# Optimization experiments

Hardware: AMD Instinct MI355X
Metric: run time of the kernel (lower is better)

Reference implementation:

```python
import jax, jax.numpy as jnp
import numpy as np

EPS = 1e-6

def rms_norm(x):
    # RMSNorm, affine=False
    return x * jax.lax.rsqrt(jnp.mean(x * x, axis=-1, keepdims=True) + EPS)

def apply_rope(x, cos, sin):
    # x: [N, T, h, d], cos/sin: [T, d//2], half-split rotation
    x1, x2 = jnp.split(x, 2, axis=-1)
    c = cos[None, :, None, :]
    s = sin[None, :, None, :]
    return jnp.concatenate([x1 * c - x2 * s, x1 * s + x2 * c], axis=-1)

def setup_inputs() -> dict:
    key = jax.random.key(0)
    k0, k1, k2 = jax.random.split(key, 3)
    N, T, D, hd = 1, 2048, 2048, 128
    input_NTD = jax.random.normal(k0, (N, T, D), jnp.float32)
    qkv_weight = jax.random.normal(k1, (3, D, D), jnp.float32) / np.sqrt(D) / 2.0
    o_weight = jax.random.normal(k2, (D, D), jnp.float32) * 0.02
    # standard 1d RoPE angle table
    pos = jnp.arange(T, dtype=jnp.float32)
    inv_freq = 1.0 / (10000.0 ** (jnp.arange(hd // 2, dtype=jnp.float32) / (hd // 2)))
    ang = pos[:, None] * inv_freq[None, :]  # [T, hd//2]
    return {
        "input_NTD": input_NTD,
        "qkv_weight": qkv_weight,
        "o_weight": o_weight,
        "cos": jnp.cos(ang),
        "sin": jnp.sin(ang),
    }

def reference(input_NTD, qkv_weight, o_weight, cos, sin):
    N, T, D = input_NTD.shape
    hd = cos.shape[-1] * 2
    h = D // hd
    w = qkv_weight.reshape(3 * D, D)
    qkv = rms_norm(input_NTD) @ w.T                      # [N, T, 3D]
    qkv = qkv.reshape(N, T, 3 * h, hd)
    q, k, v = jnp.split(qkv, 3, axis=2)                  # each [N, T, h, hd]
    q = apply_rope(rms_norm(q), cos, sin)
    k = apply_rope(rms_norm(k), cos, sin)
    scale = 1.0 / np.sqrt(hd)
    scores = jnp.einsum('nqhd,nkhd->nhqk', q, k) * scale  # [N, h, T, T]
    causal = jnp.tril(jnp.ones((T, T), bool))
    scores = jnp.where(causal[None, None], scores, -jnp.inf)
    att = jax.nn.softmax(scores, axis=-1)
    x = jnp.einsum('nhqk,nkhd->nqhd', att, v).reshape(N, T, D)
    out = input_NTD + x @ o_weight.T
    return out, k, v
```

## Files before the change

### kernel.cpp

```cpp
#include <hip/hip_runtime.h>
#include <hip/hip_bf16.h>

typedef unsigned short u16;
typedef unsigned int u32;
typedef __bf16 bf16x8 __attribute__((ext_vector_type(8)));
typedef u16 u16x8 __attribute__((ext_vector_type(8)));
typedef u16 u16x4 __attribute__((ext_vector_type(4)));
typedef float f32x4 __attribute__((ext_vector_type(4)));

#define T_SEQ 2048
#define DMODEL 2048
#define NHEAD 16
#define HDIM 128
#define ATT_SCALE 0.08838834764831843f

__device__ __forceinline__ u16 f2bf(float f) {
    return __builtin_bit_cast(u16, __float2bfloat16(f));
}
__device__ __forceinline__ bf16x8 as_bf(u16x8 v) {
    return __builtin_bit_cast(bf16x8, v);
}
__device__ __forceinline__ float lo2f(u32 w) { return __builtin_bit_cast(float, w << 16); }
__device__ __forceinline__ float hi2f(u32 w) { return __builtin_bit_cast(float, w & 0xffff0000u); }
__device__ __forceinline__ float bf2f(u16 v) { return __builtin_bit_cast(float, (u32)v << 16); }
__device__ __forceinline__ void gload_lds16(const u16* g, u16* l) {
    __builtin_amdgcn_global_load_lds(
        (const __attribute__((address_space(1))) u32*)(g),
        (__attribute__((address_space(3))) u32*)(l), 16, 0, 0);
}

__global__ __launch_bounds__(256) void prep(const float* __restrict__ w1,
                                            const float* __restrict__ w2,
                                            const float* __restrict__ x,
                                            u16* __restrict__ d1,
                                            u16* __restrict__ d2,
                                            u16* __restrict__ xn) {
    const int b = blockIdx.x, tid = threadIdx.x;
    if (b < 8192) {
        int i = b * 256 + tid;
        const float* src; u16* dst; int k;
        if (i < 1572864) { src = w1; dst = d1; k = i; }
        else             { src = w2; dst = d2; k = i - 1572864; }
        float4 a = ((const float4*)src)[2 * k];
        float4 bb = ((const float4*)src)[2 * k + 1];
        u16x8 o;
        o[0] = f2bf(a.x); o[1] = f2bf(a.y); o[2] = f2bf(a.z); o[3] = f2bf(a.w);
        o[4] = f2bf(bb.x); o[5] = f2bf(bb.y); o[6] = f2bf(bb.z); o[7] = f2bf(bb.w);
        *(u16x8*)(dst + (size_t)k * 8) = o;
        return;
    }
    const int row = b - 8192;
    const float* xr = x + (size_t)row * DMODEL;
    float4 a = ((const float4*)xr)[2 * tid];
    float4 bb = ((const float4*)xr)[2 * tid + 1];
    float ss = a.x*a.x + a.y*a.y + a.z*a.z + a.w*a.w
             + bb.x*bb.x + bb.y*bb.y + bb.z*bb.z + bb.w*bb.w;
#pragma unroll
    for (int off = 32; off; off >>= 1) ss += __shfl_xor(ss, off);
    __shared__ float red[4];
    if ((tid & 63) == 0) red[tid >> 6] = ss;
    __syncthreads();
    float tot = red[0] + red[1] + red[2] + red[3];
    float r = rsqrtf(tot * (1.f / DMODEL) + 1e-6f);
    u16x8 o;
    o[0] = f2bf(a.x*r); o[1] = f2bf(a.y*r); o[2] = f2bf(a.z*r); o[3] = f2bf(a.w*r);
    o[4] = f2bf(bb.x*r); o[5] = f2bf(bb.y*r); o[6] = f2bf(bb.z*r); o[7] = f2bf(bb.w*r);
    *(u16x8*)(xn + (size_t)row * DMODEL + tid * 8) = o;
}

#define VM2 asm volatile("s_waitcnt vmcnt(2)" ::: "memory");
#define VM4 asm volatile("s_waitcnt vmcnt(4)" ::: "memory");
#define VM0 asm volatile("s_waitcnt vmcnt(0)" ::: "memory");

#define ENDP                                                                  \
  __builtin_amdgcn_s_barrier();                                               \
  __builtin_amdgcn_sched_barrier(0);

#define LDA6(DST, BUF, MH)                                                    \
  _Pragma("unroll") for (int mq = 0; mq < 4; ++mq) {                          \
    int ra = wr + (MH) * 64 + mq * 16 + fr;                                   \
    int sw = ra & 7;                                                          \
    _Pragma("unroll") for (int k2 = 0; k2 < 2; ++k2)                          \
      DST[mq][k2] = *(const u16x8*)(sA[BUF] + ra * 64 +                       \
                                    ((((k2 << 2) | fg) ^ sw) << 3));          \
  }

#define LDB0_192(BUF)                                                         \
  _Pragma("unroll") for (int nq = 0; nq < 2; ++nq) {                          \
    int rb = wc + nq * 16 + fr;                                               \
    int sw = rb & 7;                                                          \
    _Pragma("unroll") for (int k2 = 0; k2 < 2; ++k2)                          \
      bv[nq][k2] = *(const u16x8*)(sB[BUF] + rb * 64 +                        \
                                   ((((k2 << 2) | fg) ^ sw) << 3));           \
  }

#define LDB1_192(BUF)                                                         \
  {                                                                           \
    int rb = wc + 32 + fr;                                                    \
    int sw = rb & 7;                                                          \
    _Pragma("unroll") for (int k2 = 0; k2 < 2; ++k2)                          \
      bv1[k2] = *(const u16x8*)(sB[BUF] + rb * 64 +                           \
                                ((((k2 << 2) | fg) ^ sw) << 3));              \
  }

#define MN0(AV, MH)                                                           \
  __builtin_amdgcn_s_barrier();                                               \
  __builtin_amdgcn_s_setprio(1);                                              \
  _Pragma("unroll") for (int k2 = 0; k2 < 2; ++k2)                            \
    _Pragma("unroll") for (int mq = 0; mq < 4; ++mq)                          \
      _Pragma("unroll") for (int nq = 0; nq < 2; ++nq)                        \
        acc[(MH) * 4 + mq][nq] = __builtin_amdgcn_mfma_f32_16x16x32_bf16(     \
            as_bf(AV[mq][k2]), as_bf(bv[nq][k2]), acc[(MH) * 4 + mq][nq],     \
            0, 0, 0);                                                         \
  __builtin_amdgcn_s_setprio(0);

#define MN1B                                                                  \
  __builtin_amdgcn_s_barrier();                                               \
  __builtin_amdgcn_s_setprio(1);                                              \
  _Pragma("unroll") for (int k2 = 0; k2 < 2; ++k2)                            \
    _Pragma("unroll") for (int mq = 0; mq < 4; ++mq) {                        \
      acc[mq][2] = __builtin_amdgcn_mfma_f32_16x16x32_bf16(                   \
          as_bf(av[mq][k2]), as_bf(bv1[k2]), acc[mq][2], 0, 0, 0);            \
      acc[4 + mq][2] = __builtin_amdgcn_mfma_f32_16x16x32_bf16(               \
          as_bf(av2[mq][k2]), as_bf(bv1[k2]), acc[4 + mq][2], 0, 0, 0);       \
    }                                                                         \
  __builtin_amdgcn_s_setprio(0);

__global__ __launch_bounds__(512) void gemm192(const u16* __restrict__ A,
                                               const u16* __restrict__ B,
                                               u16* __restrict__ C,
                                               int M, int N, int K) {
    extern __shared__ char smem[];
    const int tid = threadIdx.x, lane = tid & 63, wid = tid >> 6;
    const int bm = blockIdx.y * 256, bn = blockIdx.x * 192;
    const int wr = (wid >> 2) * 128, wc = (wid & 3) * 48;
    const int fr = lane & 15, fg = lane >> 4;

    u16* sA[2] = {(u16*)smem, (u16*)(smem + 57344)};
    u16* sB[2] = {(u16*)(smem + 32768), (u16*)(smem + 90112)};

    const int cs = (((tid & 7) ^ ((tid >> 3) & 7)) << 3);
    const int s8 = (tid & 7) << 3;
    const int rr6 = tid >> 3;

    auto stA = [&](int buf, int k0, int mh) {
#pragma unroll
        for (int j = 0; j < 2; ++j) {
            int r = j * 128 + mh * 64 + rr6;
            gload_lds16(A + (size_t)(bm + r) * K + k0 + cs, sA[buf] + r * 64 + s8);
        }
    };
    auto stB = [&](int buf, int k0, int bt) {
        int r = bt * 64 + rr6;
        gload_lds16(B + (size_t)(bn + r) * K + k0 + cs, sB[buf] + r * 64 + s8);
    };

    f32x4 acc[8][3] = {};
    u16x8 av[4][2], av2[4][2], bv[2][2], bv1[2];
    const int nt = K >> 6;

    stA(0, 0, 0); stA(0, 0, 1); stB(0, 0, 0); stB(0, 0, 1); stB(0, 0, 2);
    stA(1, 64, 0); stA(1, 64, 1);
    VM4
    __builtin_amdgcn_s_barrier();
    __builtin_amdgcn_sched_barrier(0);

    for (int it = 0; it < (nt >> 1); ++it) {
        const int kc = it << 7;
        const int kn1 = kc + 64, kn2 = kc + 128, kn3 = kc + 192;
        const bool st2 = (kn2 < K), st3 = (kn3 < K);

        LDA6(av, 0, 0) LDB0_192(0)
        stB(1, kn1, 0); stB(1, kn1, 1);
        MN0(av, 0) ENDP
        LDB1_192(0) LDA6(av2, 0, 1)
        stB(1, kn1, 2);
        if (st2) stA(0, kn2, 0);
        MN1B ENDP
        if (st2) stA(0, kn2, 1);
        MN0(av2, 1)
        if (st2) { VM4 } else { VM0 }
        ENDP
        LDA6(av, 1, 0) LDB0_192(1)
        if (st2) { stB(0, kn2, 0); stB(0, kn2, 1); }
        MN0(av, 0) ENDP
        LDB1_192(1) LDA6(av2, 1, 1)
        if (st2) stB(0, kn2, 2);
        if (st3) stA(1, kn3, 0);
        MN1B ENDP
        if (st3) stA(1, kn3, 1);
        MN0(av2, 1)
        if (st3) { VM4 } else { VM0 }
        ENDP
    }

#pragma unroll
    for (int am = 0; am < 8; ++am)
#pragma unroll
        for (int bq = 0; bq < 3; ++bq)
#pragma unroll
            for (int r = 0; r < 4; ++r) {
                int row = bm + wr + am * 16 + fg * 4 + r;
                int col = bn + wc + bq * 16 + fr;
                C[(size_t)row * N + col] = f2bf(acc[am][bq][r]);
            }
}

#define LDAH(BUF, MH)                                                         \
  _Pragma("unroll") for (int mq = 0; mq < 2; ++mq) {                          \
    int ra = wr + (MH) * 32 + mq * 16 + fr;                                   \
    int sw = ra & 7;                                                          \
    _Pragma("unroll") for (int k2 = 0; k2 < 2; ++k2)                          \
      avh[mq][k2] = *(const u16x8*)(sA[BUF] + ra * 64 +                       \
                                    ((((k2 << 2) | fg) ^ sw) << 3));          \
  }

#define LDBH(BUF, NH)                                                         \
  _Pragma("unroll") for (int nq = 0; nq < 2; ++nq) {                          \
    int rb = wc + (NH) * 32 + nq * 16 + fr;                                   \
    int sw = rb & 7;                                                          \
    _Pragma("unroll") for (int k2 = 0; k2 < 2; ++k2)                          \
      bvh[nq][k2] = *(const u16x8*)(sB[BUF] + rb * 64 +                       \
                                    ((((k2 << 2) | fg) ^ sw) << 3));          \
  }

#define MFMAQH(MH, NH)                                                        \
  __builtin_amdgcn_s_barrier();                                               \
  __builtin_amdgcn_s_setprio(1);                                              \
  _Pragma("unroll") for (int k2 = 0; k2 < 2; ++k2)                            \
    _Pragma("unroll") for (int mq = 0; mq < 2; ++mq)                          \
      _Pragma("unroll") for (int nq = 0; nq < 2; ++nq)                        \
        acc[(MH) * 2 + mq][(NH) * 2 + nq] =                                   \
            __builtin_amdgcn_mfma_f32_16x16x32_bf16(                          \
                as_bf(avh[mq][k2]), as_bf(bvh[nq][k2]),                       \
                acc[(MH) * 2 + mq][(NH) * 2 + nq], 0, 0, 0);                  \
  __builtin_amdgcn_s_setprio(0);

__global__ __launch_bounds__(256) void gemm128(const u16* __restrict__ A,
                                               const u16* __restrict__ B,
                                               float* __restrict__ C,
                                               const float* __restrict__ resid,
                                               int M, int N, int K) {
    extern __shared__ char smem[];
    const int tid = threadIdx.x, lane = tid & 63, wid = tid >> 6;
    const int bm = blockIdx.y * 128, bn = blockIdx.x * 128;
    const int wr = (wid >> 1) * 64, wc = (wid & 1) * 64;
    const int fr = lane & 15, fg = lane >> 4;

    u16* sA[2] = {(u16*)smem, (u16*)(smem + 32768)};
    u16* sB[2] = {(u16*)(smem + 16384), (u16*)(smem + 49152)};

    const int cs = (((tid & 7) ^ ((tid >> 3) & 7)) << 3);
    const int s8 = (tid & 7) << 3;
    const int rr5 = tid >> 3;

    auto stA = [&](int buf, int k0, int mh) {
#pragma unroll
        for (int j = 0; j < 2; ++j) {
            int r = j * 64 + mh * 32 + rr5;
            gload_lds16(A + (size_t)(bm + r) * K + k0 + cs, sA[buf] + r * 64 + s8);
        }
    };
    auto stB = [&](int buf, int k0, int nh) {
#pragma unroll
        for (int j = 0; j < 2; ++j) {
            int r = j * 64 + nh * 32 + rr5;
            gload_lds16(B + (size_t)(bn + r) * K + k0 + cs, sB[buf] + r * 64 + s8);
        }
    };

    f32x4 acc[4][4] = {};
    u16x8 avh[2][2], bvh[2][2];
    const int nt = K >> 6;

    stA(0, 0, 0); stA(0, 0, 1); stB(0, 0, 0); stB(0, 0, 1);
    stA(1, 64, 0); stB(1, 64, 1);
    VM4
    __builtin_amdgcn_s_barrier();
    __builtin_amdgcn_sched_barrier(0);

    for (int it = 0; it < (nt >> 1); ++it) {
        const int kc = it << 7;
        const int kn1 = kc + 64, kn2 = kc + 128, kn3 = kc + 192;
        const bool st2 = (kn2 < K), st3 = (kn3 < K);

        LDAH(0, 0) LDBH(0, 0)
        stA(1, kn1, 1);
        MFMAQH(0, 0) ENDP
        LDBH(0, 1)
        stB(1, kn1, 0);
        MFMAQH(0, 1) ENDP
        LDAH(0, 1)
        if (st2) stA(0, kn2, 0);
        MFMAQH(1, 1) ENDP
        LDBH(0, 0)
        if (st2) stB(0, kn2, 1);
        MFMAQH(1, 0)
        if (st2) { VM4 } else { VM0 }
        ENDP
        LDAH(1, 0) LDBH(1, 0)
        if (st2) stA(0, kn2, 1);
        MFMAQH(0, 0) ENDP
        LDBH(1, 1)
        if (st2) stB(0, kn2, 0);
        MFMAQH(0, 1) ENDP
        LDAH(1, 1)
        if (st3) stA(1, kn3, 0);
        MFMAQH(1, 1) ENDP
        LDBH(1, 0)
        if (st3) stB(1, kn3, 1);
        MFMAQH(1, 0)
        VM4
        ENDP
    }

#pragma unroll
    for (int am = 0; am < 4; ++am)
#pragma unroll
        for (int bq = 0; bq < 4; ++bq)
#pragma unroll
            for (int r = 0; r < 4; ++r) {
                int row = bm + wr + am * 16 + fg * 4 + r;
                int col = bn + wc + bq * 16 + fr;
                float val = acc[am][bq][r] + resid[(size_t)row * N + col];
                C[(size_t)row * N + col] = val;
            }
}

__global__ __launch_bounds__(256) void rope_split(const u16* __restrict__ qkv,
                                                  const float* __restrict__ cosb,
                                                  const float* __restrict__ sinb,
                                                  u16* __restrict__ q_bf,
                                                  u16* __restrict__ k_bf,
                                                  float* __restrict__ k_out,
                                                  float* __restrict__ v_out) {
    const int t = blockIdx.x, tid = threadIdx.x, wid = tid >> 6, lane = tid & 63;
    const u16* row = qkv + (size_t)t * (3 * DMODEL);
    const int dp = (lane & 31) << 1;
    float2 c2 = *(const float2*)(cosb + t * 64 + dp);
    float2 s2 = *(const float2*)(sinb + t * 64 + dp);
    const bool hi = lane >= 32;

    for (int task = wid; task < 32; task += 4) {
        u32 w = *(const u32*)(row + task * 128 + lane * 2);
        float xa = lo2f(w), xb = hi2f(w);
        float ss = xa * xa + xb * xb;
#pragma unroll
        for (int off = 32; off; off >>= 1) ss += __shfl_xor(ss, off);
        float rn = rsqrtf(ss * (1.f / 128.f) + 1e-6f);
        float pa = __shfl_xor(xa, 32), pb = __shfl_xor(xb, 32);
        float oa, ob;
        if (!hi) {
            oa = (xa * c2.x - pa * s2.x) * rn;
            ob = (xb * c2.y - pb * s2.y) * rn;
        } else {
            oa = (pa * s2.x + xa * c2.x) * rn;
            ob = (pb * s2.y + xb * c2.y) * rn;
        }
        u32 pk = (u32)f2bf(oa) | ((u32)f2bf(ob) << 16);
        if (task < 16) {
            *(u32*)(q_bf + ((size_t)task * T_SEQ + t) * 128 + lane * 2) = pk;
        } else {
            int hh = task - 16;
            *(u32*)(k_bf + ((size_t)hh * T_SEQ + t) * 128 + lane * 2) = pk;
            float2 kk; kk.x = oa; kk.y = ob;
            *(float2*)(k_out + (size_t)t * DMODEL + hh * 128 + lane * 2) = kk;
        }
    }
    {
        u16x8 vv = *(const u16x8*)(row + 2 * DMODEL + tid * 8);
        float4 f0, f1;
        f0.x = bf2f(vv[0]); f0.y = bf2f(vv[1]); f0.z = bf2f(vv[2]); f0.w = bf2f(vv[3]);
        f1.x = bf2f(vv[4]); f1.y = bf2f(vv[5]); f1.z = bf2f(vv[6]); f1.w = bf2f(vv[7]);
        *(float4*)(v_out + (size_t)t * DMODEL + tid * 8) = f0;
        *(float4*)(v_out + (size_t)t * DMODEL + tid * 8 + 4) = f1;
    }
}

__global__ __launch_bounds__(256) void vtrans(const u16* __restrict__ qkv,
                                              u16* __restrict__ vt) {
    const int b = blockIdx.x, tid = threadIdx.x;
    const int head = b >> 7;
    const int i = (b & 127) * 256 + tid;
    const int d = i & 127, tc = i >> 7;
    u16x8 o;
#pragma unroll
    for (int j = 0; j < 8; ++j)
        o[j] = qkv[(size_t)(tc * 8 + j) * (3 * DMODEL) + 2 * DMODEL + head * 128 + d];
    *(u16x8*)&vt[((size_t)head * 128 + d) * T_SEQ + tc * 8] = o;
}

__global__ __launch_bounds__(256) void attn_part(const u16* __restrict__ qb,
                                                 const u16* __restrict__ kb,
                                                 const u16* __restrict__ vtb,
                                                 u16* __restrict__ opart,
                                                 float* __restrict__ ml) {
    __shared__ u16 Ks[64 * 128];
    __shared__ u16 Vs[128 * 64];
    __shared__ u16 Ps[4][16 * 64];

    const int bid = blockIdx.x;
    const int r8 = bid & 7, s = bid >> 3;
    const int hs = s >> 6, g = (s >> 5) & 1, m = s & 31;
    const int head = r8 + (hs << 3);
    const int qt = g ? (31 - m) : m;
    const int nt = qt + 1;
    const int h0c = (nt + 1) >> 1;
    const int first = g ? h0c : 0;
    const int count = g ? (nt - h0c) : h0c;
    const int pidx = (head * 32 + qt) * 2 + g;

    const int tid = threadIdx.x, wid = tid >> 6, lane = tid & 63;
    const int fr = lane & 15, fg = lane >> 4;
    const u16* kh = kb + (size_t)head * T_SEQ * 128;
    const u16* vth = vtb + (size_t)head * 128 * T_SEQ;
    const u16* qh = qb + (size_t)head * T_SEQ * 128;
    const int q0 = qt * 64 + wid * 16;
    const int qrow_g = q0 + fr;

    u16x8 bq[4];
    {
        const u16* qrow = qh + (size_t)(q0 + fr) * 128 + fg * 8;
#pragma unroll
        for (int cc = 0; cc < 4; ++cc) bq[cc] = *(const u16x8*)(qrow + cc * 32);
    }

    auto stage = [&](int kv0) {
#pragma unroll
        for (int i = 0; i < 4; ++i) {
            int idx = i * 256 + tid;
            int r = idx >> 4;
            int cbs = ((idx & 15) << 4) ^ ((r & 7) << 4);
            gload_lds16(kh + (size_t)(kv0 + r) * 128 + (cbs >> 1), &Ks[idx * 8]);
        }
#pragma unroll
        for (int i = 0; i < 4; ++i) {
            int idx = i * 256 + tid;
            int d = idx >> 3;
            int cbs = ((idx & 7) << 4) ^ ((d & 7) << 4);
            gload_lds16(vth + (size_t)d * T_SEQ + kv0 + (cbs >> 1), &Vs[idx * 8]);
        }
    };

    f32x4 o[8] = {};
    float m_run = -1e30f, l_run = 0.f;

    for (int i = 0; i < count; ++i) {
        const int kv0 = (first + i) * 64;
        stage(kv0);
        asm volatile("s_waitcnt vmcnt(0)" ::: "memory");
        __builtin_amdgcn_s_barrier();
        __builtin_amdgcn_sched_barrier(0);

        const char* ksb = (const char*)&Ks[0];
        const char* vsb = (const char*)&Vs[0];
        char* psb = (char*)&Ps[wid][0];

        float p[4][4];
        float mx = -1e30f;
        const bool diag = (kv0 + 64 > q0);
#pragma unroll
        for (int st = 0; st < 4; ++st) {
            f32x4 sacc = {0.f, 0.f, 0.f, 0.f};
#pragma unroll
            for (int c4 = 0; c4 < 4; ++c4) {
                int r = st * 16 + fr;
                int cb = c4 * 64 + fg * 16;
                u16x8 ak = *(const u16x8*)(ksb + r * 256 + (cb ^ ((r & 7) << 4)));
                sacc = __builtin_amdgcn_mfma_f32_16x16x32_bf16(
                    as_bf(ak), as_bf(bq[c4]), sacc, 0, 0, 0);
            }
#pragma unroll
            for (int rr = 0; rr < 4; ++rr) {
                float sv = sacc[rr] * ATT_SCALE;
                if (diag) {
                    int kvg = kv0 + st * 16 + fg * 4 + rr;
                    sv = (kvg <= qrow_g) ? sv : -1e30f;
                }
                p[st][rr] = sv;
                mx = fmaxf(mx, sv);
            }
        }
        mx = fmaxf(mx, __shfl_xor(mx, 16));
        mx = fmaxf(mx, __shfl_xor(mx, 32));

        if (__all(mx - m_run <= 8.f)) {
            float rs = 0.f;
#pragma unroll
            for (int st = 0; st < 4; ++st) {
                u16x4 pw;
#pragma unroll
                for (int rr = 0; rr < 4; ++rr) {
                    float e = __expf(p[st][rr] - m_run);
                    rs += e;
                    pw[rr] = f2bf(e);
                }
                *(u16x4*)(psb + fr * 128 + ((st * 32 + fg * 8) ^ ((fr & 7) << 4))) = pw;
            }
            rs += __shfl_xor(rs, 16);
            rs += __shfl_xor(rs, 32);
            l_run += rs;
        } else {
            float m_new = fmaxf(m_run, mx);
            float corr = __expf(m_run - m_new);
            float rs = 0.f;
#pragma unroll
            for (int st = 0; st < 4; ++st) {
                u16x4 pw;
#pragma unroll
                for (int rr = 0; rr < 4; ++rr) {
                    float e = __expf(p[st][rr] - m_new);
                    rs += e;
                    pw[rr] = f2bf(e);
                }
                *(u16x4*)(psb + fr * 128 + ((st * 32 + fg * 8) ^ ((fr & 7) << 4))) = pw;
            }
            rs += __shfl_xor(rs, 16);
            rs += __shfl_xor(rs, 32);
            l_run = l_run * corr + rs;
            m_run = m_new;
            float ct[4];
#pragma unroll
            for (int rr = 0; rr < 4; ++rr) ct[rr] = __shfl(corr, fg * 4 + rr);
#pragma unroll
            for (int f = 0; f < 8; ++f)
#pragma unroll
                for (int rr = 0; rr < 4; ++rr) o[f][rr] *= ct[rr];
        }

#pragma unroll
        for (int ks = 0; ks < 2; ++ks) {
            u16x8 pa = *(const u16x8*)(psb + fr * 128 + ((ks * 64 + fg * 16) ^ ((fr & 7) << 4)));
#pragma unroll
            for (int f = 0; f < 8; ++f) {
                int d = f * 16 + fr;
                u16x8 vB = *(const u16x8*)(vsb + d * 128 + ((ks * 64 + fg * 16) ^ ((d & 7) << 4)));
                o[f] = __builtin_amdgcn_mfma_f32_16x16x32_bf16(
                    as_bf(pa), as_bf(vB), o[f], 0, 0, 0);
            }
        }
        __builtin_amdgcn_s_barrier();
        __builtin_amdgcn_sched_barrier(0);
    }

    u16* op = opart + (size_t)pidx * 8192;
#pragma unroll
    for (int f = 0; f < 8; ++f)
#pragma unroll
        for (int rr = 0; rr < 4; ++rr)
            op[(wid * 16 + fg * 4 + rr) * 128 + f * 16 + fr] = f2bf(o[f][rr]);
    if (fg == 0) {
        ml[pidx * 128 + wid * 16 + fr] = m_run;
        ml[pidx * 128 + 64 + wid * 16 + fr] = l_run;
    }
}

__global__ __launch_bounds__(256) void attn_merge(const u16* __restrict__ opart,
                                                  const float* __restrict__ ml,
                                                  u16* __restrict__ xout) {
    const int b = blockIdx.x, tid = threadIdx.x;
    const int head = b >> 5, qt = b & 31;
    const int p0 = b * 2, p1 = b * 2 + 1;
    const int row = tid >> 2, d0 = (tid & 3) * 32;

    float m0 = ml[p0 * 128 + row], l0 = ml[p0 * 128 + 64 + row];
    float m1 = ml[p1 * 128 + row], l1 = ml[p1 * 128 + 64 + row];
    float M = fmaxf(m0, m1);
    float w0 = __expf(m0 - M), w1 = __expf(m1 - M);
    float inv = 1.f / (l0 * w0 + l1 * w1);
    w0 *= inv; w1 *= inv;

    const u16* a0 = opart + (size_t)p0 * 8192 + row * 128 + d0;
    const u16* a1 = opart + (size_t)p1 * 8192 + row * 128 + d0;
    u16* dst = xout + (size_t)(qt * 64 + row) * DMODEL + head * 128 + d0;
#pragma unroll
    for (int j = 0; j < 4; ++j) {
        u16x8 v0 = *(const u16x8*)(a0 + j * 8);
        u16x8 v1 = *(const u16x8*)(a1 + j * 8);
        u16x8 ov;
#pragma unroll
        for (int e = 0; e < 8; ++e)
            ov[e] = f2bf(bf2f(v0[e]) * w0 + bf2f(v1[e]) * w1);
        *(u16x8*)(dst + j * 8) = ov;
    }
}

extern "C" void kernel_launch(void* const* d_in, const int* in_sizes, int n_in,
                              void* d_out, int out_size, void* d_ws, size_t ws_size,
                              hipStream_t stream) {
    const float* x_in = (const float*)d_in[0];
    const float* w_qkv = (const float*)d_in[1];
    const float* w_o = (const float*)d_in[2];
    const float* cosb = (const float*)d_in[3];
    const float* sinb = (const float*)d_in[4];

    float* out = (float*)d_out;
    float* k_out = out + 4194304;
    float* v_out = out + 8388608;

    char* ws = (char*)d_ws;
    u16* xn    = (u16*)(ws);
    u16* w_bf  = (u16*)(ws + (size_t)(8u << 20));
    u16* o_bf  = (u16*)(ws + (size_t)(32u << 20));
    u16* qkv   = (u16*)(ws + (size_t)(40u << 20));
    u16* q_bf  = (u16*)(ws + (size_t)(64u << 20));
    u16* k_bf  = (u16*)(ws + (size_t)(72u << 20));
    u16* vt_bf = (u16*)(ws + (size_t)(80u << 20));
    u16* x_bf  = (u16*)(ws + (size_t)(88u << 20));
    u16* opart = (u16*)(ws + (size_t)(40u << 20));
    float* mlb = (float*)(ws + (size_t)(56u << 20));

    (void)hipFuncSetAttribute(reinterpret_cast<const void*>(&gemm192),
                              hipFuncAttributeMaxDynamicSharedMemorySize, 114688);
    (void)hipFuncSetAttribute(reinterpret_cast<const void*>(&gemm128),
                              hipFuncAttributeMaxDynamicSharedMemorySize, 65536);

    prep<<<10240, 256, 0, stream>>>(w_qkv, w_o, x_in, w_bf, o_bf, xn);
    gemm192<<<dim3(32, 8), 512, 114688, stream>>>(xn, w_bf, qkv, 2048, 6144, 2048);
    rope_split<<<2048, 256, 0, stream>>>(qkv, cosb, sinb, q_bf, k_bf, k_out, v_out);
    vtrans<<<2048, 256, 0, stream>>>(qkv, vt_bf);
    attn_part<<<1024, 256, 0, stream>>>(q_bf, k_bf, vt_bf, opart, mlb);
    attn_merge<<<512, 256, 0, stream>>>(opart, mlb, x_bf);
    gemm128<<<dim3(16, 16), 256, 65536, stream>>>(x_bf, o_bf, out, x_in, 2048, 2048, 2048);
}
```

Measured before the change: 177.0 us.

## Prefetch next K/V tile into registers to overlap global loads with attention compute

The attention kernel no longer loads K/V tiles straight from global into LDS and waits on them. Each tile is now loaded into registers one iteration ahead, then written to the swizzled LDS layout at the start of the next iteration, so global latency overlaps the current tile's MFMA work. The trailing barrier is replaced by one at the top of the loop, and launch bounds now request 4 blocks per SM. The prefetch buffers cost extra VGPRs, which could cause spills under the new occupancy bound, and LDS writes now go through registers instead of direct global-to-LDS loads.

```diff
diff --git a/kernel.cpp b/kernel.cpp
--- a/kernel.cpp
+++ b/kernel.cpp
@@ -390,11 +390,11 @@
     *(u16x8*)&vt[((size_t)head * 128 + d) * T_SEQ + tc * 8] = o;
 }
 
-__global__ __launch_bounds__(256) void attn_part(const u16* __restrict__ qb,
-                                                 const u16* __restrict__ kb,
-                                                 const u16* __restrict__ vtb,
-                                                 u16* __restrict__ opart,
-                                                 float* __restrict__ ml) {
+__global__ __launch_bounds__(256, 4) void attn_part(const u16* __restrict__ qb,
+                                                    const u16* __restrict__ kb,
+                                                    const u16* __restrict__ vtb,
+                                                    u16* __restrict__ opart,
+                                                    float* __restrict__ ml) {
     __shared__ u16 Ks[64 * 128];
     __shared__ u16 Vs[128 * 64];
     __shared__ u16 Ps[4][16 * 64];
@@ -425,30 +425,43 @@
         for (int cc = 0; cc < 4; ++cc) bq[cc] = *(const u16x8*)(qrow + cc * 32);
     }
 
-    auto stage = [&](int kv0) {
+    u16x8 kr[4], vr[4];
+    auto ldregs = [&](int kv0) {
 #pragma unroll
         for (int i = 0; i < 4; ++i) {
             int idx = i * 256 + tid;
-            int r = idx >> 4;
-            int cbs = ((idx & 15) << 4) ^ ((r & 7) << 4);
-            gload_lds16(kh + (size_t)(kv0 + r) * 128 + (cbs >> 1), &Ks[idx * 8]);
+            kr[i] = *(const u16x8*)(kh + (size_t)(kv0 + (idx >> 4)) * 128 + (idx & 15) * 8);
         }
 #pragma unroll
         for (int i = 0; i < 4; ++i) {
             int idx = i * 256 + tid;
-            int d = idx >> 3;
-            int cbs = ((idx & 7) << 4) ^ ((d & 7) << 4);
-            gload_lds16(vth + (size_t)d * T_SEQ + kv0 + (cbs >> 1), &Vs[idx * 8]);
+            vr[i] = *(const u16x8*)(vth + (size_t)(idx >> 3) * T_SEQ + kv0 + (idx & 7) * 8);
         }
     };
+    int kwo[4], vwo[4];
+#pragma unroll
+    for (int i = 0; i < 4; ++i) {
+        int idx = i * 256 + tid;
+        int r = idx >> 4, c16 = idx & 15;
+        kwo[i] = r * 128 + ((c16 ^ (r & 7)) << 3);
+        int d = idx >> 3, c8 = idx & 7;
+        vwo[i] = d * 64 + ((c8 ^ (d & 7)) << 3);
+    }
+
+    if (count > 0) ldregs(first * 64);
 
     f32x4 o[8] = {};
     float m_run = -1e30f, l_run = 0.f;
 
     for (int i = 0; i < count; ++i) {
         const int kv0 = (first + i) * 64;
-        stage(kv0);
-        asm volatile("s_waitcnt vmcnt(0)" ::: "memory");
+        __builtin_amdgcn_s_barrier();
+#pragma unroll
+        for (int j = 0; j < 4; ++j) *(u16x8*)&Ks[kwo[j]] = kr[j];
+#pragma unroll
+        for (int j = 0; j < 4; ++j) *(u16x8*)&Vs[vwo[j]] = vr[j];
+        if (i + 1 < count) ldregs(kv0 + 64);
+        asm volatile("s_waitcnt lgkmcnt(0)" ::: "memory");
         __builtin_amdgcn_s_barrier();
         __builtin_amdgcn_sched_barrier(0);
 
@@ -539,7 +552,6 @@
                     as_bf(pa), as_bf(vB), o[f], 0, 0, 0);
             }
         }
-        __builtin_amdgcn_s_barrier();
         __builtin_amdgcn_sched_barrier(0);
     }
 
```

After: 340.8 us. 1.93x slower.
